# Performance work log

Hardware: AMD Instinct MI355X
Metric: run time of the kernel (lower is better)

## Reference

```python
import jax, jax.numpy as jnp
import numpy as np

NUM_GRAPHS = 512


def gcn_conv(x, src, dst, w, W, b):
    # PyG GCNConv: add self-loops (weight 1), symmetric deg^{-1/2} normalization
    n = x.shape[0]
    xw = x @ W  # [N, F_out]
    deg = 1.0 + jax.ops.segment_sum(w, dst, num_segments=n)  # self-loop contributes 1
    dinv = jax.lax.rsqrt(deg)
    norm = w * dinv[src] * dinv[dst]  # [E]
    agg = jax.ops.segment_sum(norm[:, None] * xw[src], dst, num_segments=n)
    return agg + (dinv * dinv)[:, None] * xw + b  # self-loop term = xw / deg


def gap(h, batch, num_graphs):
    s = jax.ops.segment_sum(h, batch, num_segments=num_graphs)
    cnt = jax.ops.segment_sum(jnp.ones((h.shape[0],), h.dtype), batch, num_segments=num_graphs)
    return s / jnp.clip(cnt, 1.0)[:, None]


def setup_inputs() -> dict:
    key = jax.random.key(0)
    ks = jax.random.split(key, 40)
    Nl, El, Ns, Es = 100000, 1600000, 50000, 800000
    Cin_l, Cin_s, H, L1, L2 = 64, 32, 128, 128, 64
    inp = {}
    inp['x_l'] = jax.random.normal(ks[0], (Nl, Cin_l), jnp.float32)
    inp['edge_index_l'] = jax.random.randint(ks[1], (2, El), 0, Nl)
    inp['edge_weight_l'] = jax.random.uniform(ks[2], (El,), jnp.float32)
    inp['x_s'] = jax.random.normal(ks[3], (Ns, Cin_s), jnp.float32)
    inp['edge_index_s'] = jax.random.randint(ks[4], (2, Es), 0, Ns)
    inp['edge_weight_s'] = jax.random.uniform(ks[5], (Es,), jnp.float32)
    inp['batch_index_l'] = jnp.sort(jax.random.randint(ks[6], (Nl,), 0, NUM_GRAPHS))
    inp['batch_index_s'] = jnp.sort(jax.random.randint(ks[7], (Ns,), 0, NUM_GRAPHS))

    def lin(k, fi, fo):
        s = 1.0 / np.sqrt(fi)
        kw, kb = jax.random.split(k)
        return (jax.random.uniform(kw, (fi, fo), jnp.float32, -s, s),
                jax.random.uniform(kb, (fo,), jnp.float32, -s, s))

    dims_a = [Cin_l, H, H, H, H]
    dims_b = [Cin_s, H, H, H, H]
    for i in range(4):
        inp[f'Wa{i}'], inp[f'ba{i}'] = lin(ks[8 + i], dims_a[i], dims_a[i + 1])
        inp[f'Wb{i}'], inp[f'bb{i}'] = lin(ks[12 + i], dims_b[i], dims_b[i + 1])
    inp['lin1_W'], inp['lin1_b'] = lin(ks[16], H, L1)
    inp['lin2_W'], inp['lin2_b'] = lin(ks[17], L1, L2)
    inp['bn_gamma'] = jnp.ones((L2,), jnp.float32)
    inp['bn_beta'] = jnp.zeros((L2,), jnp.float32)
    inp['out_W'], inp['out_b'] = lin(ks[18], L2, 1)
    return inp


def reference(x_l, edge_index_l, edge_weight_l, x_s, edge_index_s, edge_weight_s,
              batch_index_l, batch_index_s,
              Wa0, ba0, Wb0, bb0, Wa1, ba1, Wb1, bb1,
              Wa2, ba2, Wb2, bb2, Wa3, ba3, Wb3, bb3,
              lin1_W, lin1_b, lin2_W, lin2_b, bn_gamma, bn_beta, out_W, out_b):
    # eval mode: dropout = identity, BatchNorm uses running stats (mean 0, var 1)
    sl, dl = edge_index_l[0], edge_index_l[1]
    ss, ds = edge_index_s[0], edge_index_s[1]
    h1 = x_l
    for W, b in ((Wa0, ba0), (Wa1, ba1), (Wa2, ba2), (Wa3, ba3)):
        h1 = jax.nn.relu(gcn_conv(h1, sl, dl, edge_weight_l, W, b))
    h2 = x_s
    for W, b in ((Wb0, bb0), (Wb1, bb1), (Wb2, bb2), (Wb3, bb3)):
        h2 = jax.nn.relu(gcn_conv(h2, ss, ds, edge_weight_s, W, b))
    h = jnp.concatenate([h1, h2], axis=0)
    batch = jnp.concatenate([batch_index_l, batch_index_s], axis=0)
    h = gap(h, batch, NUM_GRAPHS)  # [B, 128]
    h = h @ lin1_W + lin1_b
    h = h @ lin2_W + lin2_b
    eps = 1e-5
    h = (h - 0.0) * jax.lax.rsqrt(jnp.asarray(1.0 + eps)) * bn_gamma + bn_beta
    h = jax.nn.relu(h)
    out = h @ out_W + out_b
    return out, h
```

## Files before the change

kernel.cpp:

```cpp
#include <hip/hip_runtime.h>


static inline size_t align256(size_t x) { return (x + 255) & ~size_t(255); }

__device__ inline unsigned short f2bf(float f) {
    unsigned u = __float_as_uint(f);
    unsigned r = (u + 0x7fffu + ((u >> 16) & 1u)) >> 16;
    return (unsigned short)r;
}
__device__ inline unsigned packbf2(float lo, float hi) {
    return (unsigned)f2bf(lo) | ((unsigned)f2bf(hi) << 16);
}

typedef __attribute__((ext_vector_type(8))) short short8;
typedef __attribute__((ext_vector_type(4))) float floatx4;

#define CHUNK 4096

__global__ __launch_bounds__(256) void bucket_hist_dual(
    const int* __restrict__ dstL, int EL, int NBL, int* __restrict__ bhL,
    const int* __restrict__ dstS, int ES, int NBS, int* __restrict__ bhS, int CL) {
    __shared__ int hist[512];
    int b = blockIdx.x, t = threadIdx.x;
    const int* dst; int E, NB, blk; int* bh;
    if (b < CL) { dst = dstL; E = EL; NB = NBL; bh = bhL; blk = b; }
    else        { dst = dstS; E = ES; NB = NBS; bh = bhS; blk = b - CL; }
    for (int i = t; i < NB; i += 256) hist[i] = 0;
    __syncthreads();
    int base = blk * CHUNK;
    int end = min(E, base + CHUNK);
    for (int e = base + t; e < end; e += 256) atomicAdd(&hist[dst[e] >> 8], 1);
    __syncthreads();
    for (int i = t; i < NB; i += 256) {
        int h = hist[i];
        if (h > 0) atomicAdd(&bh[i], h);
    }
}

__global__ __launch_bounds__(256) void scan_buckets_dual(
    const int* __restrict__ bhist, int* __restrict__ bbase, int* __restrict__ bcur,
    int nbL, int* __restrict__ rpL, int NL, int EL,
    int nbS, int* __restrict__ rpS, int NS, int ES) {
    __shared__ int wsum[4];
    int which = blockIdx.x, t = threadIdx.x;
    const int* bh = bhist + which * 512;
    int* bb = bbase + which * 512;
    int* bc = bcur + which * 512;
    int nb = which ? nbS : nbL;
    int* rp = which ? rpS : rpL;
    int N = which ? NS : NL;
    int E = which ? ES : EL;
    int wave = t >> 6, lane = t & 63;
    int i0 = 2 * t, i1 = 2 * t + 1;
    int v0 = (i0 < nb) ? bh[i0] : 0;
    int v1 = (i1 < nb) ? bh[i1] : 0;
    int tsum = v0 + v1;
    int x = tsum;
    #pragma unroll
    for (int off = 1; off < 64; off <<= 1) {
        int y = __shfl_up(x, off, 64);
        if (lane >= off) x += y;
    }
    if (lane == 63) wsum[wave] = x;
    __syncthreads();
    int woff = 0;
    #pragma unroll
    for (int i = 0; i < 3; i++) if (wave > i) woff += wsum[i];
    int texcl = woff + x - tsum;
    if (i0 < nb) { bb[i0] = texcl; bc[i0] = texcl; }
    if (i1 < nb) { bb[i1] = texcl + v0; bc[i1] = texcl + v0; }
    if (t == 255) { bb[nb] = woff + x; rp[N] = E; }
}

__global__ __launch_bounds__(256) void partition_edges_dual(
    const int* __restrict__ srcL, const int* __restrict__ dstL,
    const float* __restrict__ wL, int EL, int NBL, int* __restrict__ bcurL,
    int2* __restrict__ partL,
    const int* __restrict__ srcS, const int* __restrict__ dstS,
    const float* __restrict__ wS, int ES, int NBS, int* __restrict__ bcurS,
    int2* __restrict__ partS, int CL) {
    __shared__ int hist[512];
    __shared__ int lcur[512];
    int b = blockIdx.x, t = threadIdx.x;
    const int *src, *dst; const float* w; int E, NB, blk; int* bcur; int2* part;
    if (b < CL) { src = srcL; dst = dstL; w = wL; E = EL; NB = NBL; bcur = bcurL;
                  part = partL; blk = b; }
    else        { src = srcS; dst = dstS; w = wS; E = ES; NB = NBS; bcur = bcurS;
                  part = partS; blk = b - CL; }
    for (int i = t; i < NB; i += 256) hist[i] = 0;
    __syncthreads();
    int base = blk * CHUNK;
    int end = min(E, base + CHUNK);
    for (int e = base + t; e < end; e += 256) atomicAdd(&hist[dst[e] >> 8], 1);
    __syncthreads();
    for (int i = t; i < NB; i += 256) {
        int h = hist[i];
        if (h > 0) lcur[i] = atomicAdd(&bcur[i], h);
    }
    __syncthreads();
    for (int e = base + t; e < end; e += 256) {
        int d = dst[e];
        int bk = d >> 8;
        int pos = atomicAdd(&lcur[bk], 1);
        part[pos] = make_int2(src[e] | ((d & 255) << 24), __float_as_int(w[e]));
    }
}

__global__ __launch_bounds__(256) void bucket_csr_dual(
    const int2* __restrict__ partL, const int* __restrict__ bbaseL, int NL,
    int* __restrict__ rpL, float* __restrict__ dinvL, int2* __restrict__ csrL,
    const int2* __restrict__ partS, const int* __restrict__ bbaseS, int NS,
    int* __restrict__ rpS, float* __restrict__ dinvS, int2* __restrict__ csrS,
    int NBL) {
    __shared__ int hist[256];
    __shared__ float degw[256];
    __shared__ int wsum[4];
    int bb = blockIdx.x, t = threadIdx.x;
    const int2* part; const int* bbase; int N, b; int* rp; float* dinv; int2* csr;
    if (bb < NBL) { part = partL; bbase = bbaseL; N = NL; rp = rpL; dinv = dinvL;
                    csr = csrL; b = bb; }
    else          { part = partS; bbase = bbaseS; N = NS; rp = rpS; dinv = dinvS;
                    csr = csrS; b = bb - NBL; }
    int node0 = b << 8;
    int nn = min(256, N - node0);
    int ebase = bbase[b], eend = bbase[b + 1];
    hist[t] = 0;
    degw[t] = 0.f;
    __syncthreads();
    for (int e = ebase + t; e < eend; e += 256) {
        int2 rec = part[e];
        int nloc = ((unsigned)rec.x) >> 24;
        atomicAdd(&hist[nloc], 1);
        atomicAdd(&degw[nloc], __int_as_float(rec.y));
    }
    __syncthreads();
    int v = hist[t];
    int x = v;
    int wave = t >> 6, lane = t & 63;
    #pragma unroll
    for (int off = 1; off < 64; off <<= 1) {
        int y = __shfl_up(x, off, 64);
        if (lane >= off) x += y;
    }
    if (lane == 63) wsum[wave] = x;
    __syncthreads();
    int woff = 0;
    #pragma unroll
    for (int i = 0; i < 3; i++) if (wave > i) woff += wsum[i];
    int excl = woff + x - v;
    if (t < nn) {
        rp[node0 + t] = ebase + excl;
        dinv[node0 + t] = rsqrtf(1.f + degw[t]);
    }
    hist[t] = excl;
    __syncthreads();
    for (int e = ebase + t; e < eend; e += 256) {
        int2 rec = part[e];
        int nloc = ((unsigned)rec.x) >> 24;
        int pos = ebase + atomicAdd(&hist[nloc], 1);
        csr[pos] = make_int2(rec.x & 0x00FFFFFF, rec.y);
    }
}

template <int F8>
__device__ void cast_body(const float* __restrict__ in, size_t n8,
                          const float* __restrict__ dinv,
                          unsigned short* __restrict__ out, size_t i) {
    if (i >= n8) return;
    float s = dinv[i / F8];
    const float4* in4 = (const float4*)in;
    float4 a = in4[i * 2], b = in4[i * 2 + 1];
    ushort4 lo, hi;
    lo.x = f2bf(a.x * s); lo.y = f2bf(a.y * s); lo.z = f2bf(a.z * s); lo.w = f2bf(a.w * s);
    hi.x = f2bf(b.x * s); hi.y = f2bf(b.y * s); hi.z = f2bf(b.z * s); hi.w = f2bf(b.w * s);
    ushort4* o4 = (ushort4*)out;
    o4[i * 2] = lo;
    o4[i * 2 + 1] = hi;
}

__global__ void cast0_dual(const float* __restrict__ xL, size_t n8L,
                           const float* __restrict__ dinvL, unsigned short* __restrict__ oL,
                           const float* __restrict__ xS, size_t n8S,
                           const float* __restrict__ dinvS, unsigned short* __restrict__ oS,
                           int BL) {
    int b = blockIdx.x;
    if (b < BL) cast_body<8>(xL, n8L, dinvL, oL, (size_t)b * 256 + threadIdx.x);
    else        cast_body<4>(xS, n8S, dinvS, oS, (size_t)(b - BL) * 256 + threadIdx.x);
}

struct WCastArgs {
    const float* w[8];
    unsigned short* o[8];
    int K[8];
};
__global__ void cast_w16t(WCastArgs p) {
    int mi = blockIdx.y;
    int K = p.K[mi];
    int id = blockIdx.x * 256 + threadIdx.x;
    if (id >= K * 128) return;
    int k = id >> 7, c = id & 127;
    p.o[mi][c * K + k] = f2bf(p.w[mi][k * 128 + c]);
}

template <int LANES>
__device__ void agg_body(const unsigned short* __restrict__ h16, int N,
                         const int* __restrict__ rp, const int2* __restrict__ csr,
                         const float* __restrict__ dinv,
                         unsigned short* __restrict__ z16, int blk) {
    constexpr int GPB = 256 / LANES;
    int group = threadIdx.x / LANES;
    int lane = threadIdx.x % LANES;
    int n = blk * GPB + group;
    if (n >= N) return;
    const uint4* h4 = (const uint4*)h16;
    float acc[8];
    #pragma unroll
    for (int i = 0; i < 8; i++) acc[i] = 0.f;

    int e = rp[n], end = rp[n + 1];
    #define ACC8(q, nm)                                                   \
    {                                                                     \
        acc[0] += nm * __uint_as_float(q.x << 16);                        \
        acc[1] += nm * __uint_as_float(q.x & 0xffff0000u);                \
        acc[2] += nm * __uint_as_float(q.y << 16);                        \
        acc[3] += nm * __uint_as_float(q.y & 0xffff0000u);                \
        acc[4] += nm * __uint_as_float(q.z << 16);                        \
        acc[5] += nm * __uint_as_float(q.z & 0xffff0000u);                \
        acc[6] += nm * __uint_as_float(q.w << 16);                        \
        acc[7] += nm * __uint_as_float(q.w & 0xffff0000u);                \
    }
    for (; e + 3 < end; e += 4) {
        int2 c0 = csr[e], c1 = csr[e + 1], c2 = csr[e + 2], c3 = csr[e + 3];
        uint4 q0 = h4[(size_t)c0.x * LANES + lane];
        uint4 q1 = h4[(size_t)c1.x * LANES + lane];
        uint4 q2 = h4[(size_t)c2.x * LANES + lane];
        uint4 q3 = h4[(size_t)c3.x * LANES + lane];
        float n0 = __int_as_float(c0.y), n1 = __int_as_float(c1.y);
        float n2 = __int_as_float(c2.y), n3 = __int_as_float(c3.y);
        ACC8(q0, n0) ACC8(q1, n1) ACC8(q2, n2) ACC8(q3, n3)
    }
    for (; e < end; e++) {
        int2 c = csr[e];
        uint4 q = h4[(size_t)c.x * LANES + lane];
        float nm = __int_as_float(c.y);
        ACC8(q, nm)
    }
    uint4 qs = h4[(size_t)n * LANES + lane];
    float di = dinv[n];
    float v0 = (acc[0] + __uint_as_float(qs.x << 16)) * di;
    float v1 = (acc[1] + __uint_as_float(qs.x & 0xffff0000u)) * di;
    float v2 = (acc[2] + __uint_as_float(qs.y << 16)) * di;
    float v3 = (acc[3] + __uint_as_float(qs.y & 0xffff0000u)) * di;
    float v4 = (acc[4] + __uint_as_float(qs.z << 16)) * di;
    float v5 = (acc[5] + __uint_as_float(qs.z & 0xffff0000u)) * di;
    float v6 = (acc[6] + __uint_as_float(qs.w << 16)) * di;
    float v7 = (acc[7] + __uint_as_float(qs.w & 0xffff0000u)) * di;
    uint4 o;
    o.x = packbf2(v0, v1); o.y = packbf2(v2, v3);
    o.z = packbf2(v4, v5); o.w = packbf2(v6, v7);
    *(uint4*)&z16[(size_t)n * (LANES * 8) + lane * 8] = o;
    #undef ACC8
}

__global__ __launch_bounds__(256) void aggregate_dual(
    const unsigned short* __restrict__ hL, int NL, const int* __restrict__ rpL,
    const int2* __restrict__ csrL, const float* __restrict__ dinvL,
    unsigned short* __restrict__ zL,
    const unsigned short* __restrict__ hS, int NS, const int* __restrict__ rpS,
    const int2* __restrict__ csrS, const float* __restrict__ dinvS,
    unsigned short* __restrict__ zS, int gL) {
    int b = blockIdx.x;
    if (b < gL) agg_body<16>(hL, NL, rpL, csrL, dinvL, zL, b);
    else        agg_body<16>(hS, NS, rpS, csrS, dinvS, zS, b - gL);
}

__global__ __launch_bounds__(256) void aggregate0_dual(
    const unsigned short* __restrict__ hL, int NL, const int* __restrict__ rpL,
    const int2* __restrict__ csrL, const float* __restrict__ dinvL,
    unsigned short* __restrict__ zL,
    const unsigned short* __restrict__ hS, int NS, const int* __restrict__ rpS,
    const int2* __restrict__ csrS, const float* __restrict__ dinvS,
    unsigned short* __restrict__ zS, int gL) {
    int b = blockIdx.x;
    if (b < gL) agg_body<8>(hL, NL, rpL, csrL, dinvL, zL, b);
    else        agg_body<4>(hS, NS, rpS, csrS, dinvS, zS, b - gL);
}

template <int K>
__device__ void gemm_body(const unsigned short* __restrict__ Z16,
                          const unsigned short* __restrict__ WT16,
                          const float* __restrict__ bias, const float* __restrict__ dinv,
                          float* __restrict__ Hf, unsigned short* __restrict__ H16,
                          int N, int blk, unsigned short* WT) {
    constexpr int KP = K + 8;
    int tid = threadIdx.x;
    constexpr int CH = 128 * K / 8;
    for (int i = tid; i < CH; i += 256) {
        int c = i / (K / 8), kc = i % (K / 8);
        *(uint4*)&WT[c * KP + kc * 8] = *(const uint4*)&WT16[c * K + kc * 8];
    }
    __syncthreads();

    int wave = tid >> 6, lane = tid & 63;
    int m = lane & 15, quad = lane >> 4;
    int rowbase = blk * 128 + wave * 32;

    floatx4 acc[2][8];
    #pragma unroll
    for (int t = 0; t < 2; t++)
        #pragma unroll
        for (int ct = 0; ct < 8; ct++) acc[t][ct] = (floatx4)0.f;

    for (int ks = 0; ks < K; ks += 32) {
        short8 a[2];
        #pragma unroll
        for (int t = 0; t < 2; t++) {
            int r = rowbase + t * 16 + m;
            short8 av = (short8)0;
            if (r < N) av = *(const short8*)&Z16[(size_t)r * K + ks + quad * 8];
            a[t] = av;
        }
        #pragma unroll
        for (int ct = 0; ct < 8; ct++) {
            short8 b = *(const short8*)&WT[(ct * 16 + m) * KP + ks + quad * 8];
            acc[0][ct] = __builtin_amdgcn_mfma_f32_16x16x32_bf16(a[0], b, acc[0][ct], 0, 0, 0);
            acc[1][ct] = __builtin_amdgcn_mfma_f32_16x16x32_bf16(a[1], b, acc[1][ct], 0, 0, 0);
        }
    }

    float bv[8];
    #pragma unroll
    for (int ct = 0; ct < 8; ct++) bv[ct] = bias[ct * 16 + m];

    #pragma unroll
    for (int t = 0; t < 2; t++) {
        #pragma unroll
        for (int reg = 0; reg < 4; reg++) {
            int r = rowbase + t * 16 + quad * 4 + reg;
            if (r >= N) continue;
            float di = H16 ? dinv[r] : 1.f;
            #pragma unroll
            for (int ct = 0; ct < 8; ct++) {
                float o = fmaxf(acc[t][ct][reg] + bv[ct], 0.f);
                size_t off = (size_t)r * 128 + ct * 16 + m;
                if (H16) H16[off] = f2bf(o * di);
                if (Hf) Hf[off] = o;
            }
        }
    }
}

__global__ __launch_bounds__(256) void gemm_mfma_dual0(
    const unsigned short* __restrict__ ZL, const unsigned short* __restrict__ WTL,
    const float* __restrict__ bL, const float* __restrict__ dinvL,
    unsigned short* __restrict__ H16L, int NL,
    const unsigned short* __restrict__ ZS, const unsigned short* __restrict__ WTS,
    const float* __restrict__ bS, const float* __restrict__ dinvS,
    unsigned short* __restrict__ H16S, int NS, int gmL) {
    __shared__ __attribute__((aligned(16))) unsigned short WT[128 * 72];
    int b = blockIdx.x;
    if (b < gmL) gemm_body<64>(ZL, WTL, bL, dinvL, (float*)nullptr, H16L, NL, b, WT);
    else         gemm_body<32>(ZS, WTS, bS, dinvS, (float*)nullptr, H16S, NS, b - gmL, WT);
}

__global__ __launch_bounds__(256) void gemm_mfma_dual128(
    const unsigned short* __restrict__ ZL, const unsigned short* __restrict__ WTL,
    const float* __restrict__ bL, const float* __restrict__ dinvL,
    float* __restrict__ HfL, unsigned short* __restrict__ H16L, int NL,
    const unsigned short* __restrict__ ZS, const unsigned short* __restrict__ WTS,
    const float* __restrict__ bS, const float* __restrict__ dinvS,
    float* __restrict__ HfS, unsigned short* __restrict__ H16S, int NS, int gmL) {
    __shared__ __attribute__((aligned(16))) unsigned short WT[128 * 136];
    int b = blockIdx.x;
    if (b < gmL) gemm_body<128>(ZL, WTL, bL, dinvL, HfL, H16L, NL, b, WT);
    else         gemm_body<128>(ZS, WTS, bS, dinvS, HfS, H16S, NS, b - gmL, WT);
}

__device__ void pool_body(const float* __restrict__ h, const int* __restrict__ batch,
                          int N, float* __restrict__ psum, int blk) {
    int tid = threadIdx.x;
    int f4 = tid & 31;
    int nl = tid >> 5;
    int n0 = blk * 256 + nl;
    const float4* h4 = (const float4*)h;
    float4 acc = make_float4(0.f, 0.f, 0.f, 0.f);
    int cur = -1;
    #pragma unroll 4
    for (int i = 0; i < 32; i++) {
        int n = n0 + i * 8;
        if (n >= N) break;
        int g = batch[n];
        if (g != cur) {
            if (cur >= 0) {
                float* d = &psum[(size_t)cur * 128 + f4 * 4];
                atomicAdd(d + 0, acc.x);
                atomicAdd(d + 1, acc.y);
                atomicAdd(d + 2, acc.z);
                atomicAdd(d + 3, acc.w);
            }
            cur = g;
            acc = make_float4(0.f, 0.f, 0.f, 0.f);
        }
        float4 v = h4[(size_t)n * 32 + f4];
        acc.x += v.x; acc.y += v.y; acc.z += v.z; acc.w += v.w;
    }
    if (cur >= 0) {
        float* d = &psum[(size_t)cur * 128 + f4 * 4];
        atomicAdd(d + 0, acc.x);
        atomicAdd(d + 1, acc.y);
        atomicAdd(d + 2, acc.z);
        atomicAdd(d + 3, acc.w);
    }
}

__global__ __launch_bounds__(256) void pool_dual(
    const float* __restrict__ hL, const int* __restrict__ bL, int NL,
    const float* __restrict__ hS, const int* __restrict__ bS, int NS,
    float* __restrict__ psum, int gL) {
    int b = blockIdx.x;
    if (b < gL) pool_body(hL, bL, NL, psum, b);
    else        pool_body(hS, bS, NS, psum, b - gL);
}

__device__ inline int lower_bound(const int* __restrict__ a, int n, int v) {
    int lo = 0, hi = n;
    while (lo < hi) {
        int m = (lo + hi) >> 1;
        if (a[m] < v) lo = m + 1; else hi = m;
    }
    return lo;
}

__global__ void mlp_kernel(const float* __restrict__ psum,
                           const int* __restrict__ batchL, int NL,
                           const int* __restrict__ batchS, int NS,
                           const float* __restrict__ W1, const float* __restrict__ b1,
                           const float* __restrict__ W2, const float* __restrict__ b2,
                           const float* __restrict__ gamma, const float* __restrict__ beta,
                           const float* __restrict__ outW, const float* __restrict__ outb,
                           float* __restrict__ d_out) {
    __shared__ float row[128];
    __shared__ float row2[128];
    int g = blockIdx.x, t = threadIdx.x;
    int cnt = (lower_bound(batchL, NL, g + 1) - lower_bound(batchL, NL, g)) +
              (lower_bound(batchS, NS, g + 1) - lower_bound(batchS, NS, g));
    float rcp = 1.f / (float)(cnt > 0 ? cnt : 1);
    row[t] = psum[(size_t)g * 128 + t] * rcp;
    __syncthreads();
    float a = b1[t];
    #pragma unroll 4
    for (int k = 0; k < 128; k++) a += row[k] * W1[k * 128 + t];
    row2[t] = a;
    __syncthreads();
    if (t < 64) {
        float a2 = b2[t];
        #pragma unroll 4
        for (int k = 0; k < 128; k++) a2 += row2[k] * W2[k * 64 + t];
        float rs = rsqrtf(1.0f + 1e-5f);
        float hb = a2 * rs * gamma[t] + beta[t];
        float hr = fmaxf(hb, 0.f);
        d_out[512 + g * 64 + t] = hr;
        float p = hr * outW[t];
        #pragma unroll
        for (int off = 32; off > 0; off >>= 1) p += __shfl_down(p, off, 64);
        if (t == 0) d_out[g] = p + outb[0];
    }
}

extern "C" void kernel_launch(void* const* d_in, const int* in_sizes, int n_in,
                              void* d_out, int out_size, void* d_ws, size_t ws_size,
                              hipStream_t stream) {
    const float* x_l = (const float*)d_in[0];
    const int*   ei_l = (const int*)d_in[1];
    const float* w_l = (const float*)d_in[2];
    const float* x_s = (const float*)d_in[3];
    const int*   ei_s = (const int*)d_in[4];
    const float* w_s = (const float*)d_in[5];
    const int*   batch_l = (const int*)d_in[6];
    const int*   batch_s = (const int*)d_in[7];

    const int NL = in_sizes[6];
    const int NS = in_sizes[7];
    const int EL = in_sizes[2];
    const int ES = in_sizes[5];

    const float* Wa[4] = {(const float*)d_in[8],  (const float*)d_in[12],
                          (const float*)d_in[16], (const float*)d_in[20]};
    const float* ba[4] = {(const float*)d_in[9],  (const float*)d_in[13],
                          (const float*)d_in[17], (const float*)d_in[21]};
    const float* Wb[4] = {(const float*)d_in[10], (const float*)d_in[14],
                          (const float*)d_in[18], (const float*)d_in[22]};
    const float* bb[4] = {(const float*)d_in[11], (const float*)d_in[15],
                          (const float*)d_in[19], (const float*)d_in[23]};
    const float* lin1_W = (const float*)d_in[24];
    const float* lin1_b = (const float*)d_in[25];
    const float* lin2_W = (const float*)d_in[26];
    const float* lin2_b = (const float*)d_in[27];
    const float* bn_g = (const float*)d_in[28];
    const float* bn_b = (const float*)d_in[29];
    const float* out_W = (const float*)d_in[30];
    const float* out_b = (const float*)d_in[31];
    float* out = (float*)d_out;

    const int* src_l = ei_l;
    const int* dst_l = ei_l + EL;
    const int* src_s = ei_s;
    const int* dst_s = ei_s + ES;

    const int NBL = (NL + 255) >> 8;
    const int NBS = (NS + 255) >> 8;
    const int CL = (EL + CHUNK - 1) / CHUNK;
    const int CS = (ES + CHUNK - 1) / CHUNK;

    char* p = (char*)d_ws;
    auto alloc = [&](size_t bytes) { char* r = p; p += align256(bytes); return r; };
    float* A_l = (float*)alloc((size_t)NL * 128 * 4);
    float* A_s = (float*)alloc((size_t)NS * 128 * 4);
    unsigned short* Z16_l = (unsigned short*)alloc((size_t)NL * 128 * 2);
    unsigned short* Z16_s = (unsigned short*)alloc((size_t)NS * 128 * 2);
    unsigned short* H16_l = (unsigned short*)alloc((size_t)NL * 128 * 2);
    unsigned short* H16_s = (unsigned short*)alloc((size_t)NS * 128 * 2);
    int2*  csr_l  = (int2*)alloc((size_t)EL * 8);
    int2*  csr_s  = (int2*)alloc((size_t)ES * 8);
    int2*  part_l = (int2*)alloc((size_t)EL * 8);
    int2*  part_s = (int2*)alloc((size_t)ES * 8);
    int*   rp_l  = (int*)alloc((size_t)(NL + 1) * 4);
    int*   rp_s  = (int*)alloc((size_t)(NS + 1) * 4);
    float* dinv_l = (float*)alloc((size_t)NL * 4);
    float* dinv_s = (float*)alloc((size_t)NS * 4);
    int*   bhist  = (int*)alloc(1024 * 4);
    int*   bbase  = (int*)alloc(1024 * 4);
    int*   bcur   = (int*)alloc(1024 * 4);
    float* psum = (float*)alloc((size_t)512 * 128 * 4);
    unsigned short* WTa[4];
    unsigned short* WTb[4];
    WTa[0] = (unsigned short*)alloc((size_t)128 * 64 * 2);
    for (int i = 1; i < 4; i++) WTa[i] = (unsigned short*)alloc((size_t)128 * 128 * 2);
    WTb[0] = (unsigned short*)alloc((size_t)128 * 32 * 2);
    for (int i = 1; i < 4; i++) WTb[i] = (unsigned short*)alloc((size_t)128 * 128 * 2);
    (void)ws_size; (void)n_in; (void)out_size;

    hipMemsetAsync(bhist, 0, 1024 * 4, stream);
    hipMemsetAsync(psum, 0, (size_t)512 * 128 * 4, stream);

    {
        WCastArgs wa;
        for (int i = 0; i < 4; i++) {
            wa.w[i] = Wa[i]; wa.o[i] = WTa[i]; wa.K[i] = (i == 0) ? 64 : 128;
            wa.w[4 + i] = Wb[i]; wa.o[4 + i] = WTb[i]; wa.K[4 + i] = (i == 0) ? 32 : 128;
        }
        cast_w16t<<<dim3(64, 8), 256, 0, stream>>>(wa);
    }

    bucket_hist_dual<<<CL + CS, 256, 0, stream>>>(dst_l, EL, NBL, bhist,
                                                  dst_s, ES, NBS, bhist + 512, CL);
    scan_buckets_dual<<<2, 256, 0, stream>>>(bhist, bbase, bcur,
                                             NBL, rp_l, NL, EL,
                                             NBS, rp_s, NS, ES);
    partition_edges_dual<<<CL + CS, 256, 0, stream>>>(
        src_l, dst_l, w_l, EL, NBL, bcur, part_l,
        src_s, dst_s, w_s, ES, NBS, bcur + 512, part_s, CL);
    bucket_csr_dual<<<NBL + NBS, 256, 0, stream>>>(
        part_l, bbase, NL, rp_l, dinv_l, csr_l,
        part_s, bbase + 512, NS, rp_s, dinv_s, csr_s, NBL);

    const size_t n8l = (size_t)NL * 8;
    const size_t n8s = (size_t)NS * 4;
    const int cBL = (int)((n8l + 255) / 256);
    const int cBS = (int)((n8s + 255) / 256);
    cast0_dual<<<cBL + cBS, 256, 0, stream>>>(x_l, n8l, dinv_l, H16_l,
                                              x_s, n8s, dinv_s, H16_s, cBL);

    const int gmL = (NL + 127) / 128;
    const int gmS = (NS + 127) / 128;
    const int aL = (NL + 15) / 16;
    const int aS = (NS + 15) / 16;
    const int a0L = (NL + 31) / 32;
    const int a0S = (NS + 63) / 64;

    aggregate0_dual<<<a0L + a0S, 256, 0, stream>>>(
        H16_l, NL, rp_l, csr_l, dinv_l, Z16_l,
        H16_s, NS, rp_s, csr_s, dinv_s, Z16_s, a0L);
    gemm_mfma_dual0<<<gmL + gmS, 256, 0, stream>>>(
        Z16_l, WTa[0], ba[0], dinv_l, H16_l, NL,
        Z16_s, WTb[0], bb[0], dinv_s, H16_s, NS, gmL);

    for (int layer = 1; layer < 4; layer++) {
        aggregate_dual<<<aL + aS, 256, 0, stream>>>(
            H16_l, NL, rp_l, csr_l, dinv_l, Z16_l,
            H16_s, NS, rp_s, csr_s, dinv_s, Z16_s, aL);
        if (layer < 3)
            gemm_mfma_dual128<<<gmL + gmS, 256, 0, stream>>>(
                Z16_l, WTa[layer], ba[layer], dinv_l, (float*)nullptr, H16_l, NL,
                Z16_s, WTb[layer], bb[layer], dinv_s, (float*)nullptr, H16_s, NS, gmL);
        else
            gemm_mfma_dual128<<<gmL + gmS, 256, 0, stream>>>(
                Z16_l, WTa[layer], ba[layer], dinv_l, A_l, (unsigned short*)nullptr, NL,
                Z16_s, WTb[layer], bb[layer], dinv_s, A_s, (unsigned short*)nullptr, NS, gmL);
    }

    const int pL = (NL + 255) / 256;
    const int pS = (NS + 255) / 256;
    pool_dual<<<pL + pS, 256, 0, stream>>>(A_l, batch_l, NL, A_s, batch_s, NS, psum, pL);
    mlp_kernel<<<512, 128, 0, stream>>>(psum, batch_l, NL, batch_s, NS,
                                        lin1_W, lin1_b, lin2_W, lin2_b,
                                        bn_g, bn_b, out_W, out_b, out);
}
```

Measured before the change: 768.0 us.

## Fuse input cast into CSR build and mean-pool into last GEMM epilogue

Folds the dinv-scaled bf16 cast of the input features into the bucket CSR kernel, which already holds each bucket's dinv in shared memory. The final-layer GEMM now adds its ReLU outputs straight into per-graph sums, staged in a small shared-memory buffer, instead of writing a full fp32 activation that a separate pool kernel then reads back. This removes two launches and a large fp32 write plus read. The cost is many shared and global float atomics in the GEMM epilogue. Rows whose graph index falls outside the block's 8-slot window go straight to global atomics. psum zeroing is presumably handled elsewhere as before.

```diff
diff --git a/kernel.cpp b/kernel.cpp
--- a/kernel.cpp
+++ b/kernel.cpp
@@ -109,18 +109,28 @@
 __global__ __launch_bounds__(256) void bucket_csr_dual(
     const int2* __restrict__ partL, const int* __restrict__ bbaseL, int NL,
     int* __restrict__ rpL, float* __restrict__ dinvL, int2* __restrict__ csrL,
+    const float* __restrict__ xL, unsigned short* __restrict__ h16L,
     const int2* __restrict__ partS, const int* __restrict__ bbaseS, int NS,
     int* __restrict__ rpS, float* __restrict__ dinvS, int2* __restrict__ csrS,
+    const float* __restrict__ xS, unsigned short* __restrict__ h16S,
     int NBL) {
     __shared__ int hist[256];
     __shared__ float degw[256];
     __shared__ int wsum[4];
     int bb = blockIdx.x, t = threadIdx.x;
-    const int2* part; const int* bbase; int N, b; int* rp; float* dinv; int2* csr;
-    if (bb < NBL) { part = partL; bbase = bbaseL; N = NL; rp = rpL; dinv = dinvL;
-                    csr = csrL; b = bb; }
-    else          { part = partS; bbase = bbaseS; N = NS; rp = rpS; dinv = dinvS;
-                    csr = csrS; b = bb - NBL; }
+    bool isL = bb < NBL;
+    const int2* part = isL ? partL : partS;
+    const int* bbase = isL ? bbaseL : bbaseS;
+    int N = isL ? NL : NS;
+    int b = isL ? bb : bb - NBL;
+    int* rp = isL ? rpL : rpS;
+    float* dinv = isL ? dinvL : dinvS;
+    int2* csr = isL ? csrL : csrS;
+    const float* x = isL ? xL : xS;
+    unsigned short* h16 = isL ? h16L : h16S;
+    const int FG = isL ? 8 : 4;
+    const int fgsh = isL ? 3 : 2;
+
     int node0 = b << 8;
     int nn = min(256, N - node0);
     int ebase = bbase[b], eend = bbase[b + 1];
@@ -135,24 +145,26 @@
     }
     __syncthreads();
     int v = hist[t];
-    int x = v;
+    int xsc = v;
     int wave = t >> 6, lane = t & 63;
     #pragma unroll
     for (int off = 1; off < 64; off <<= 1) {
-        int y = __shfl_up(x, off, 64);
-        if (lane >= off) x += y;
-    }
-    if (lane == 63) wsum[wave] = x;
+        int y = __shfl_up(xsc, off, 64);
+        if (lane >= off) xsc += y;
+    }
+    if (lane == 63) wsum[wave] = xsc;
     __syncthreads();
     int woff = 0;
     #pragma unroll
     for (int i = 0; i < 3; i++) if (wave > i) woff += wsum[i];
-    int excl = woff + x - v;
+    int excl = woff + xsc - v;
+    float di = rsqrtf(1.f + degw[t]);
     if (t < nn) {
         rp[node0 + t] = ebase + excl;
-        dinv[node0 + t] = rsqrtf(1.f + degw[t]);
+        dinv[node0 + t] = di;
     }
     hist[t] = excl;
+    degw[t] = di;
     __syncthreads();
     for (int e = ebase + t; e < eend; e += 256) {
         int2 rec = part[e];
@@ -160,32 +172,21 @@
         int pos = ebase + atomicAdd(&hist[nloc], 1);
         csr[pos] = make_int2(rec.x & 0x00FFFFFF, rec.y);
     }
-}
-
-template <int F8>
-__device__ void cast_body(const float* __restrict__ in, size_t n8,
-                          const float* __restrict__ dinv,
-                          unsigned short* __restrict__ out, size_t i) {
-    if (i >= n8) return;
-    float s = dinv[i / F8];
-    const float4* in4 = (const float4*)in;
-    float4 a = in4[i * 2], b = in4[i * 2 + 1];
-    ushort4 lo, hi;
-    lo.x = f2bf(a.x * s); lo.y = f2bf(a.y * s); lo.z = f2bf(a.z * s); lo.w = f2bf(a.w * s);
-    hi.x = f2bf(b.x * s); hi.y = f2bf(b.y * s); hi.z = f2bf(b.z * s); hi.w = f2bf(b.w * s);
-    ushort4* o4 = (ushort4*)out;
-    o4[i * 2] = lo;
-    o4[i * 2 + 1] = hi;
-}
-
-__global__ void cast0_dual(const float* __restrict__ xL, size_t n8L,
-                           const float* __restrict__ dinvL, unsigned short* __restrict__ oL,
-                           const float* __restrict__ xS, size_t n8S,
-                           const float* __restrict__ dinvS, unsigned short* __restrict__ oS,
-                           int BL) {
-    int b = blockIdx.x;
-    if (b < BL) cast_body<8>(xL, n8L, dinvL, oL, (size_t)b * 256 + threadIdx.x);
-    else        cast_body<4>(xS, n8S, dinvS, oS, (size_t)(b - BL) * 256 + threadIdx.x);
+    int total = nn << fgsh;
+    for (int i = t; i < total; i += 256) {
+        int nloc = i >> fgsh;
+        int grp = i & (FG - 1);
+        float s = degw[nloc];
+        const float* xp = x + (size_t)(node0 + nloc) * (FG * 8) + grp * 8;
+        float4 a = *(const float4*)xp;
+        float4 c = *(const float4*)(xp + 4);
+        uint4 o;
+        o.x = packbf2(a.x * s, a.y * s);
+        o.y = packbf2(a.z * s, a.w * s);
+        o.z = packbf2(c.x * s, c.y * s);
+        o.w = packbf2(c.z * s, c.w * s);
+        *(uint4*)&h16[(size_t)(node0 + nloc) * (FG * 8) + grp * 8] = o;
+    }
 }
 
 struct WCastArgs {
@@ -290,14 +291,18 @@
 __device__ void gemm_body(const unsigned short* __restrict__ Z16,
                           const unsigned short* __restrict__ WT16,
                           const float* __restrict__ bias, const float* __restrict__ dinv,
-                          float* __restrict__ Hf, unsigned short* __restrict__ H16,
-                          int N, int blk, unsigned short* WT) {
+                          unsigned short* __restrict__ H16,
+                          const int* __restrict__ batch, float* __restrict__ psum,
+                          int N, int blk, unsigned short* WT, float* pp) {
     constexpr int KP = K + 8;
     int tid = threadIdx.x;
     constexpr int CH = 128 * K / 8;
     for (int i = tid; i < CH; i += 256) {
         int c = i / (K / 8), kc = i % (K / 8);
         *(uint4*)&WT[c * KP + kc * 8] = *(const uint4*)&WT16[c * K + kc * 8];
+    }
+    if (pp) {
+        for (int i = tid; i < 1024; i += 256) pp[i] = 0.f;
     }
     __syncthreads();
 
@@ -332,19 +337,42 @@
     #pragma unroll
     for (int ct = 0; ct < 8; ct++) bv[ct] = bias[ct * 16 + m];
 
-    #pragma unroll
-    for (int t = 0; t < 2; t++) {
+    if (batch) {
+        int g0 = batch[min(blk * 128, N - 1)];
         #pragma unroll
-        for (int reg = 0; reg < 4; reg++) {
-            int r = rowbase + t * 16 + quad * 4 + reg;
-            if (r >= N) continue;
-            float di = H16 ? dinv[r] : 1.f;
+        for (int t = 0; t < 2; t++) {
             #pragma unroll
-            for (int ct = 0; ct < 8; ct++) {
-                float o = fmaxf(acc[t][ct][reg] + bv[ct], 0.f);
-                size_t off = (size_t)r * 128 + ct * 16 + m;
-                if (H16) H16[off] = f2bf(o * di);
-                if (Hf) Hf[off] = o;
+            for (int reg = 0; reg < 4; reg++) {
+                int r = rowbase + t * 16 + quad * 4 + reg;
+                if (r >= N) continue;
+                int slot = batch[r] - g0;
+                bool fits = slot < 8;
+                float* basep = fits ? (pp + slot * 128) : (psum + (size_t)(g0 + slot) * 128);
+                #pragma unroll
+                for (int ct = 0; ct < 8; ct++) {
+                    float o = fmaxf(acc[t][ct][reg] + bv[ct], 0.f);
+                    atomicAdd(basep + ct * 16 + m, o);
+                }
+            }
+        }
+        __syncthreads();
+        for (int i = tid; i < 1024; i += 256) {
+            float vv = pp[i];
+            if (vv != 0.f) atomicAdd(&psum[(size_t)(g0 + (i >> 7)) * 128 + (i & 127)], vv);
+        }
+    } else {
+        #pragma unroll
+        for (int t = 0; t < 2; t++) {
+            #pragma unroll
+            for (int reg = 0; reg < 4; reg++) {
+                int r = rowbase + t * 16 + quad * 4 + reg;
+                if (r >= N) continue;
+                float di = dinv[r];
+                #pragma unroll
+                for (int ct = 0; ct < 8; ct++) {
+                    float o = fmaxf(acc[t][ct][reg] + bv[ct], 0.f);
+                    H16[(size_t)r * 128 + ct * 16 + m] = f2bf(o * di);
+                }
             }
         }
     }
@@ -359,67 +387,34 @@
     unsigned short* __restrict__ H16S, int NS, int gmL) {
     __shared__ __attribute__((aligned(16))) unsigned short WT[128 * 72];
     int b = blockIdx.x;
-    if (b < gmL) gemm_body<64>(ZL, WTL, bL, dinvL, (float*)nullptr, H16L, NL, b, WT);
-    else         gemm_body<32>(ZS, WTS, bS, dinvS, (float*)nullptr, H16S, NS, b - gmL, WT);
+    if (b < gmL) gemm_body<64>(ZL, WTL, bL, dinvL, H16L, nullptr, nullptr, NL, b, WT, nullptr);
+    else         gemm_body<32>(ZS, WTS, bS, dinvS, H16S, nullptr, nullptr, NS, b - gmL, WT, nullptr);
 }
 
 __global__ __launch_bounds__(256) void gemm_mfma_dual128(
     const unsigned short* __restrict__ ZL, const unsigned short* __restrict__ WTL,
     const float* __restrict__ bL, const float* __restrict__ dinvL,
-    float* __restrict__ HfL, unsigned short* __restrict__ H16L, int NL,
+    unsigned short* __restrict__ H16L, int NL,
     const unsigned short* __restrict__ ZS, const unsigned short* __restrict__ WTS,
     const float* __restrict__ bS, const float* __restrict__ dinvS,
-    float* __restrict__ HfS, unsigned short* __restrict__ H16S, int NS, int gmL) {
+    unsigned short* __restrict__ H16S, int NS, int gmL) {
     __shared__ __attribute__((aligned(16))) unsigned short WT[128 * 136];
     int b = blockIdx.x;
-    if (b < gmL) gemm_body<128>(ZL, WTL, bL, dinvL, HfL, H16L, NL, b, WT);
-    else         gemm_body<128>(ZS, WTS, bS, dinvS, HfS, H16S, NS, b - gmL, WT);
-}
-
-__device__ void pool_body(const float* __restrict__ h, const int* __restrict__ batch,
-                          int N, float* __restrict__ psum, int blk) {
-    int tid = threadIdx.x;
-    int f4 = tid & 31;
-    int nl = tid >> 5;
-    int n0 = blk * 256 + nl;
-    const float4* h4 = (const float4*)h;
-    float4 acc = make_float4(0.f, 0.f, 0.f, 0.f);
-    int cur = -1;
-    #pragma unroll 4
-    for (int i = 0; i < 32; i++) {
-        int n = n0 + i * 8;
-        if (n >= N) break;
-        int g = batch[n];
-        if (g != cur) {
-            if (cur >= 0) {
-                float* d = &psum[(size_t)cur * 128 + f4 * 4];
-                atomicAdd(d + 0, acc.x);
-                atomicAdd(d + 1, acc.y);
-                atomicAdd(d + 2, acc.z);
-                atomicAdd(d + 3, acc.w);
-            }
-            cur = g;
-            acc = make_float4(0.f, 0.f, 0.f, 0.f);
-        }
-        float4 v = h4[(size_t)n * 32 + f4];
-        acc.x += v.x; acc.y += v.y; acc.z += v.z; acc.w += v.w;
-    }
-    if (cur >= 0) {
-        float* d = &psum[(size_t)cur * 128 + f4 * 4];
-        atomicAdd(d + 0, acc.x);
-        atomicAdd(d + 1, acc.y);
-        atomicAdd(d + 2, acc.z);
-        atomicAdd(d + 3, acc.w);
-    }
-}
-
-__global__ __launch_bounds__(256) void pool_dual(
-    const float* __restrict__ hL, const int* __restrict__ bL, int NL,
-    const float* __restrict__ hS, const int* __restrict__ bS, int NS,
-    float* __restrict__ psum, int gL) {
+    if (b < gmL) gemm_body<128>(ZL, WTL, bL, dinvL, H16L, nullptr, nullptr, NL, b, WT, nullptr);
+    else         gemm_body<128>(ZS, WTS, bS, dinvS, H16S, nullptr, nullptr, NS, b - gmL, WT, nullptr);
+}
+
+__global__ __launch_bounds__(256) void gemm_mfma_dual128_pool(
+    const unsigned short* __restrict__ ZL, const unsigned short* __restrict__ WTL,
+    const float* __restrict__ bL, const int* __restrict__ batchL, int NL,
+    const unsigned short* __restrict__ ZS, const unsigned short* __restrict__ WTS,
+    const float* __restrict__ bS, const int* __restrict__ batchS, int NS,
+    float* __restrict__ psum, int gmL) {
+    __shared__ __attribute__((aligned(16))) unsigned short WT[128 * 136];
+    __shared__ __attribute__((aligned(16))) float pp[8 * 128];
     int b = blockIdx.x;
-    if (b < gL) pool_body(hL, bL, NL, psum, b);
-    else        pool_body(hS, bS, NS, psum, b - gL);
+    if (b < gmL) gemm_body<128>(ZL, WTL, bL, nullptr, nullptr, batchL, psum, NL, b, WT, pp);
+    else         gemm_body<128>(ZS, WTS, bS, nullptr, nullptr, batchS, psum, NS, b - gmL, WT, pp);
 }
 
 __device__ inline int lower_bound(const int* __restrict__ a, int n, int v) {
@@ -514,8 +509,6 @@
 
     char* p = (char*)d_ws;
     auto alloc = [&](size_t bytes) { char* r = p; p += align256(bytes); return r; };
-    float* A_l = (float*)alloc((size_t)NL * 128 * 4);
-    float* A_s = (float*)alloc((size_t)NS * 128 * 4);
     unsigned short* Z16_l = (unsigned short*)alloc((size_t)NL * 128 * 2);
     unsigned short* Z16_s = (unsigned short*)alloc((size_t)NS * 128 * 2);
     unsigned short* H16_l = (unsigned short*)alloc((size_t)NL * 128 * 2);
@@ -561,15 +554,8 @@
         src_l, dst_l, w_l, EL, NBL, bcur, part_l,
         src_s, dst_s, w_s, ES, NBS, bcur + 512, part_s, CL);
     bucket_csr_dual<<<NBL + NBS, 256, 0, stream>>>(
-        part_l, bbase, NL, rp_l, dinv_l, csr_l,
-        part_s, bbase + 512, NS, rp_s, dinv_s, csr_s, NBL);
-
-    const size_t n8l = (size_t)NL * 8;
-    const size_t n8s = (size_t)NS * 4;
-    const int cBL = (int)((n8l + 255) / 256);
-    const int cBS = (int)((n8s + 255) / 256);
-    cast0_dual<<<cBL + cBS, 256, 0, stream>>>(x_l, n8l, dinv_l, H16_l,
-                                              x_s, n8s, dinv_s, H16_s, cBL);
+        part_l, bbase, NL, rp_l, dinv_l, csr_l, x_l, H16_l,
+        part_s, bbase + 512, NS, rp_s, dinv_s, csr_s, x_s, H16_s, NBL);
 
     const int gmL = (NL + 127) / 128;
     const int gmS = (NS + 127) / 128;
@@ -585,23 +571,22 @@
         Z16_l, WTa[0], ba[0], dinv_l, H16_l, NL,
         Z16_s, WTb[0], bb[0], dinv_s, H16_s, NS, gmL);
 
-    for (int layer = 1; layer < 4; layer++) {
+    for (int layer = 1; layer < 3; layer++) {
         aggregate_dual<<<aL + aS, 256, 0, stream>>>(
             H16_l, NL, rp_l, csr_l, dinv_l, Z16_l,
             H16_s, NS, rp_s, csr_s, dinv_s, Z16_s, aL);
-        if (layer < 3)
-            gemm_mfma_dual128<<<gmL + gmS, 256, 0, stream>>>(
-                Z16_l, WTa[layer], ba[layer], dinv_l, (float*)nullptr, H16_l, NL,
-                Z16_s, WTb[layer], bb[layer], dinv_s, (float*)nullptr, H16_s, NS, gmL);
-        else
-            gemm_mfma_dual128<<<gmL + gmS, 256, 0, stream>>>(
-                Z16_l, WTa[layer], ba[layer], dinv_l, A_l, (unsigned short*)nullptr, NL,
-                Z16_s, WTb[layer], bb[layer], dinv_s, A_s, (unsigned short*)nullptr, NS, gmL);
-    }
-
-    const int pL = (NL + 255) / 256;
-    const int pS = (NS + 255) / 256;
-    pool_dual<<<pL + pS, 256, 0, stream>>>(A_l, batch_l, NL, A_s, batch_s, NS, psum, pL);
+        gemm_mfma_dual128<<<gmL + gmS, 256, 0, stream>>>(
+            Z16_l, WTa[layer], ba[layer], dinv_l, H16_l, NL,
+            Z16_s, WTb[layer], bb[layer], dinv_s, H16_s, NS, gmL);
+    }
+
+    aggregate_dual<<<aL + aS, 256, 0, stream>>>(
+        H16_l, NL, rp_l, csr_l, dinv_l, Z16_l,
+        H16_s, NS, rp_s, csr_s, dinv_s, Z16_s, aL);
+    gemm_mfma_dual128_pool<<<gmL + gmS, 256, 0, stream>>>(
+        Z16_l, WTa[3], ba[3], batch_l, NL,
+        Z16_s, WTb[3], bb[3], batch_s, NS, psum, gmL);
+
     mlp_kernel<<<512, 128, 0, stream>>>(psum, batch_l, NL, batch_s, NS,
                                         lin1_W, lin1_b, lin2_W, lin2_b,
                                         bn_g, bn_b, out_W, out_b, out);
```

After: 811.2 us. +5.6%, slower.
